# Kernel optimization log

Hardware: AMD Instinct MI355X
Metric: run time of the kernel (lower is better)

Reference implementation:

```python
import jax, jax.numpy as jnp
import numpy as np
import math

B, N, L = 1, 256, 384
D_MSA, D_PAIR, H, DH = 256, 128, 8, 32
EPS = 1e-5


def layernorm(x, g, b):
    mu = jnp.mean(x, axis=-1, keepdims=True)
    var = jnp.mean(jnp.square(x - mu), axis=-1, keepdims=True)
    return (x - mu) * jax.lax.rsqrt(var + EPS) * g + b


def setup_inputs() -> dict:
    key = jax.random.key(0)
    ks = jax.random.split(key, 16)
    s_msa = 1.0 / math.sqrt(D_MSA)
    s_pair = 1.0 / math.sqrt(D_PAIR)
    s_hd = 1.0 / math.sqrt(H * DH)
    return {
        "msa": jax.random.normal(ks[0], (B, N, L, D_MSA), jnp.float32),
        "pair": jax.random.normal(ks[1], (B, L, L, D_PAIR), jnp.float32),
        "ln_msa_g": jnp.ones((D_MSA,), jnp.float32),
        "ln_msa_b": jnp.zeros((D_MSA,), jnp.float32),
        "ln_pair_g": jnp.ones((D_PAIR,), jnp.float32),
        "ln_pair_b": jnp.zeros((D_PAIR,), jnp.float32),
        # SequenceWeight projections (stored as (in, out): y = x @ W + b)
        "Wq_sw": jax.random.normal(ks[2], (D_MSA, H * DH), jnp.float32) * s_msa,
        "bq_sw": jnp.zeros((H * DH,), jnp.float32),
        "Wk_sw": jax.random.normal(ks[3], (D_MSA, H * DH), jnp.float32) * s_msa,
        "bk_sw": jnp.zeros((H * DH,), jnp.float32),
        # Main attention projections (bias-free q/k/v)
        "Wq": jax.random.normal(ks[4], (D_MSA, H * DH), jnp.float32) * s_msa,
        "Wk": jax.random.normal(ks[5], (D_MSA, H * DH), jnp.float32) * s_msa,
        "Wv": jax.random.normal(ks[6], (D_MSA, H * DH), jnp.float32) * s_msa,
        "Wb": jax.random.normal(ks[7], (D_PAIR, H), jnp.float32) * s_pair,
        "Wg": jax.random.normal(ks[8], (D_MSA, H * DH), jnp.float32) * s_msa,
        "bg": jnp.ones((H * DH,), jnp.float32),
        "Wo": jax.random.normal(ks[9], (H * DH, D_MSA), jnp.float32) * s_hd,
        "bo": jnp.zeros((D_MSA,), jnp.float32),
    }


def reference(msa, pair, ln_msa_g, ln_msa_b, ln_pair_g, ln_pair_b,
              Wq_sw, bq_sw, Wk_sw, bk_sw, Wq, Wk, Wv, Wb, Wg, bg, Wo, bo):
    b, n, l, _ = msa.shape
    scale = 1.0 / math.sqrt(DH)

    m = layernorm(msa, ln_msa_g, ln_msa_b)  # (B,N,L,d_msa)

    # --- SequenceWeight: per-sequence, per-position, per-head weights ---
    q_sw = (m[:, 0] @ Wq_sw + bq_sw).reshape(b, l, H, DH) * scale   # (B,L,h,d)
    k_sw = (m @ Wk_sw + bk_sw).reshape(b, n, l, H, DH)              # (B,N,L,h,d)
    sw_logits = jnp.einsum('bihd,bnihd->bnih', q_sw, k_sw)
    seq_weight = jax.nn.softmax(sw_logits, axis=1)[..., None]       # (B,N,L,h,1)

    # --- Row attention with pair bias ---
    q = (m @ Wq).reshape(b, n, l, H, DH) * seq_weight               # seq-weighted queries
    k = (m @ Wk).reshape(b, n, l, H, DH) * scale
    logits = jnp.einsum('bnihd,bnjhd->bijh', q, k)                  # sum over N and d
    bias = layernorm(pair, ln_pair_g, ln_pair_b) @ Wb               # (B,L,L,h)
    attn = jax.nn.softmax(logits + bias, axis=2)                    # softmax over j

    v = (m @ Wv).reshape(b, n, l, H, DH)
    out = jnp.einsum('bijh,bnjhd->bnihd', attn, v).reshape(b, n, l, H * DH)

    gate = jax.nn.sigmoid(m @ Wg + bg)
    return (out * gate) @ Wo + bo                                   # (B,N,L,d_msa)
```

## Files before the change

### kernel.cpp

```cpp
#include <hip/hip_runtime.h>
#include <stdint.h>

#define NSEQ 256
#define LRES 384
#define NH   8
#define NL   (NSEQ*LRES)
#define SCALE 0.17677669529663687f

typedef unsigned short u16;
typedef unsigned int   u32;
typedef short bf16x8 __attribute__((ext_vector_type(8)));
typedef float f32x4  __attribute__((ext_vector_type(4)));

__device__ __forceinline__ u16 f2bf(float f) {
    u32 x = __float_as_uint(f);
    return (u16)((x + 0x7fffu + ((x >> 16) & 1u)) >> 16);
}
__device__ __forceinline__ u32 pack2(float a, float b) {
    u32 xa = __float_as_uint(a);
    u32 xb = __float_as_uint(b);
    xa = (xa + 0x7fffu + ((xa >> 16) & 1u)) >> 16;
    xb = ((xb + 0x7fffu + ((xb >> 16) & 1u)) >> 16) << 16;
    return xa | xb;
}
__device__ __forceinline__ uint4 pack8(const float f[8]) {
    uint4 r;
    r.x = pack2(f[0], f[1]); r.y = pack2(f[2], f[3]);
    r.z = pack2(f[4], f[5]); r.w = pack2(f[6], f[7]);
    return r;
}
__device__ __forceinline__ void unpack2(u32 u, float& f0, float& f1) {
    f0 = __uint_as_float((u & 0xffffu) << 16);
    f1 = __uint_as_float(u & 0xffff0000u);
}
__device__ __forceinline__ void unpack8(uint4 p, float f[8]) {
    unpack2(p.x, f[0], f[1]);
    unpack2(p.y, f[2], f[3]);
    unpack2(p.z, f[4], f[5]);
    unpack2(p.w, f[6], f[7]);
}

__device__ __forceinline__ float wred_sum(float v) {
#pragma unroll
    for (int o = 32; o > 0; o >>= 1) v += __shfl_xor(v, o, 64);
    return v;
}
__device__ __forceinline__ float wred_max(float v) {
#pragma unroll
    for (int o = 32; o > 0; o >>= 1) v = fmaxf(v, __shfl_xor(v, o, 64));
    return v;
}

__global__ __launch_bounds__(256) void ln_msa_k(
    const float* __restrict__ x, const float* __restrict__ g,
    const float* __restrict__ b, u16* __restrict__ lnA,
    float* __restrict__ stats)
{
    const int lane = threadIdx.x & 63;
    const int row = blockIdx.x * 4 + (threadIdx.x >> 6);
    const size_t base = (size_t)row * 256 + lane * 4;
    float4 v = *(const float4*)(x + base);
    float s  = wred_sum(v.x + v.y + v.z + v.w);
    float sq = wred_sum(v.x*v.x + v.y*v.y + v.z*v.z + v.w*v.w);
    const float mu  = s * (1.f / 256.f);
    const float var = sq * (1.f / 256.f) - mu * mu;
    const float rs  = rsqrtf(var + 1e-5f);
    if (lane == 0) {
        stats[(size_t)row * 2]     = mu;
        stats[(size_t)row * 2 + 1] = rs;
    }
    float4 gg = *(const float4*)(g + lane * 4);
    float4 bb = *(const float4*)(b + lane * 4);
    float f0 = (v.x - mu) * rs * gg.x + bb.x;
    float f1 = (v.y - mu) * rs * gg.y + bb.y;
    float f2 = (v.z - mu) * rs * gg.z + bb.z;
    float f3 = (v.w - mu) * rs * gg.w + bb.w;
    uint2 pk;
    pk.x = pack2(f0, f1);
    pk.y = pack2(f2, f3);
    *(uint2*)(lnA + base) = pk;
}

__global__ __launch_bounds__(256) void wconv_k(
    const float* __restrict__ W0, const float* __restrict__ W1,
    const float* __restrict__ W2, const float* __restrict__ W3,
    const float* __restrict__ W4, const float* __restrict__ W5,
    u16* __restrict__ outAll)
{
    const float* Wsrc[6] = {W0, W1, W2, W3, W4, W5};
    const int widx = blockIdx.x >> 4;
    const int tile = blockIdx.x & 15;
    const int kt = tile >> 2, ct = tile & 3;
    const float* W = Wsrc[widx];
    __shared__ float ts[64][65];
    const int r  = threadIdx.x >> 2;
    const int cg = threadIdx.x & 3;
#pragma unroll
    for (int jj = 0; jj < 4; ++jj) {
        float4 v = *(const float4*)(W + (size_t)(kt * 64 + r) * 256
                                      + ct * 64 + cg * 16 + jj * 4);
        ts[r][cg * 16 + jj * 4 + 0] = v.x;
        ts[r][cg * 16 + jj * 4 + 1] = v.y;
        ts[r][cg * 16 + jj * 4 + 2] = v.z;
        ts[r][cg * 16 + jj * 4 + 3] = v.w;
    }
    __syncthreads();
    float lo[8], hi[8];
#pragma unroll
    for (int j = 0; j < 8; ++j) lo[j] = ts[cg * 16 + j][r];
#pragma unroll
    for (int j = 0; j < 8; ++j) hi[j] = ts[cg * 16 + 8 + j][r];
    u16* o = outAll + (size_t)widx * 65536 + (size_t)(ct * 64 + r) * 256
           + kt * 64 + cg * 16;
    *(uint4*)(o)     = pack8(lo);
    *(uint4*)(o + 8) = pack8(hi);
}

__global__ __launch_bounds__(128) void wbprep_k(
    const float* __restrict__ g, const float* __restrict__ b,
    const float* __restrict__ Wb, float* __restrict__ Wp,
    float* __restrict__ AB)
{
    __shared__ float ps[128][8];
    __shared__ float pb[128][8];
    const int c = threadIdx.x;
    const float gc = g[c], bc = b[c];
    float4 w0 = *(const float4*)(Wb + (size_t)c * 8);
    float4 w1 = *(const float4*)(Wb + (size_t)c * 8 + 4);
    const float wraw[8] = {w0.x, w0.y, w0.z, w0.w, w1.x, w1.y, w1.z, w1.w};
    float wp[8];
#pragma unroll
    for (int h = 0; h < 8; ++h) {
        wp[h] = wraw[h] * gc;
        ps[c][h] = wp[h];
        pb[c][h] = wraw[h] * bc;
    }
    *(float4*)(Wp + (size_t)c * 8)     = make_float4(wp[0], wp[1], wp[2], wp[3]);
    *(float4*)(Wp + (size_t)c * 8 + 4) = make_float4(wp[4], wp[5], wp[6], wp[7]);
    __syncthreads();
    if (c < 8) {
        float a = 0.f;
        for (int j = 0; j < 128; ++j) a += ps[j][c];
        AB[c] = a;
    } else if (c < 16) {
        const int h = c - 8;
        float a = 0.f;
        for (int j = 0; j < 128; ++j) a += pb[j][h];
        AB[8 + h] = a;
    }
}

__global__ __launch_bounds__(256) void gemm_ln_k(
    const void* __restrict__ Av, int a_bf16,
    const float* __restrict__ stats,
    const float* __restrict__ lng, const float* __restrict__ lnb,
    const float* __restrict__ W, const float* __restrict__ bias,
    void* __restrict__ out, const float* __restrict__ seqw, int mode)
{
    __shared__ float As_t[32][68];
    __shared__ float Ws[32][132];
    __shared__ float gs[256], bs[256];
    const int tid = threadIdx.x;
    const int bx = blockIdx.y;
    const int by = blockIdx.x;
    const int tx = tid & 15, ty = tid >> 4;
    const int ar = tid >> 2, acg = tid & 3;
    const int wr = tid >> 3, wcg = tid & 7;
    const bool do_ln = (stats != nullptr);

    if (do_ln) { gs[tid] = lng[tid]; bs[tid] = lnb[tid]; }
    __syncthreads();

    const int arow_idx = by * 64 + ar;
    float mu = 0.f, rsg = 0.f;
    if (do_ln) {
        mu  = stats[(size_t)arow_idx * 2];
        rsg = stats[(size_t)arow_idx * 2 + 1];
    }

    float acc[4][8];
#pragma unroll
    for (int i = 0; i < 4; ++i)
#pragma unroll
        for (int j = 0; j < 8; ++j) acc[i][j] = 0.f;

    const size_t arow = (size_t)arow_idx * 256 + acg * 8;

    for (int kk = 0; kk < 256; kk += 32) {
        float af[8];
        if (a_bf16) {
            uint4 a8 = *(const uint4*)((const u16*)Av + arow + kk);
            unpack8(a8, af);
        } else {
            float4 x0 = *(const float4*)((const float*)Av + arow + kk);
            float4 x1 = *(const float4*)((const float*)Av + arow + kk + 4);
            af[0] = x0.x; af[1] = x0.y; af[2] = x0.z; af[3] = x0.w;
            af[4] = x1.x; af[5] = x1.y; af[6] = x1.z; af[7] = x1.w;
        }
        const float* wrow = W + (size_t)(kk + wr) * 256 + bx * 128 + wcg * 16;
        float4 w0 = *(const float4*)(wrow);
        float4 w1 = *(const float4*)(wrow + 4);
        float4 w2 = *(const float4*)(wrow + 8);
        float4 w3 = *(const float4*)(wrow + 12);
        if (do_ln) {
#pragma unroll
            for (int j = 0; j < 8; ++j) {
                const int k = kk + acg * 8 + j;
                af[j] = (af[j] - mu) * rsg * gs[k] + bs[k];
            }
        }
        __syncthreads();
#pragma unroll
        for (int j = 0; j < 8; ++j) As_t[acg * 8 + j][ar] = af[j];
        float* wsrow = &Ws[wr][wcg * 16];
        *(float4*)(wsrow)      = w0;
        *(float4*)(wsrow + 4)  = w1;
        *(float4*)(wsrow + 8)  = w2;
        *(float4*)(wsrow + 12) = w3;
        __syncthreads();
#pragma unroll 8
        for (int k = 0; k < 32; ++k) {
            const float4 a  = *(const float4*)&As_t[k][ty * 4];
            const float4 b0 = *(const float4*)&Ws[k][tx * 8];
            const float4 b1 = *(const float4*)&Ws[k][tx * 8 + 4];
            const float av[4] = {a.x, a.y, a.z, a.w};
            const float bv[8] = {b0.x, b0.y, b0.z, b0.w, b1.x, b1.y, b1.z, b1.w};
#pragma unroll
            for (int i = 0; i < 4; ++i)
#pragma unroll
                for (int j = 0; j < 8; ++j)
                    acc[i][j] = fmaf(av[i], bv[j], acc[i][j]);
        }
    }

    const int gc0 = bx * 128 + tx * 8;
    float bias8[8];
#pragma unroll
    for (int j = 0; j < 8; ++j) bias8[j] = bias[gc0 + j];

    float* o = (float*)out;
#pragma unroll
    for (int i = 0; i < 4; ++i) {
        const size_t gr = (size_t)by * 64 + ty * 4 + i;
#pragma unroll
        for (int j = 0; j < 8; ++j)
            o[gr * 256 + gc0 + j] = (acc[i][j] + bias8[j]) * SCALE;
    }
}

__global__ __launch_bounds__(256) void softmax_n_k(float* __restrict__ swl)
{
    const int col = blockIdx.x * 4 + (threadIdx.x >> 6);
    const int lane = threadIdx.x & 63;
    float* base = swl + col;
    float v[4];
#pragma unroll
    for (int t = 0; t < 4; ++t) v[t] = base[(size_t)(lane * 4 + t) * 3072];
    float mx = wred_max(fmaxf(fmaxf(v[0], v[1]), fmaxf(v[2], v[3])));
    float e[4], s = 0.f;
#pragma unroll
    for (int t = 0; t < 4; ++t) { e[t] = __expf(v[t] - mx); s += e[t]; }
    s = wred_sum(s);
    const float inv = 1.f / s;
#pragma unroll
    for (int t = 0; t < 4; ++t) base[(size_t)(lane * 4 + t) * 3072] = e[t] * inv;
}

__global__ __launch_bounds__(256) void pair_bias_k(
    const float* __restrict__ pairX, const float* __restrict__ Wp,
    const float* __restrict__ AB, float* __restrict__ biasH)
{
    __shared__ float ws[128][8];
    __shared__ float As[8], Bs[8];
    const int tid = threadIdx.x;
    {
        float4 w4 = *(const float4*)(Wp + tid * 4);
        *(float4*)(&ws[tid >> 1][(tid & 1) * 4]) = w4;
    }
    if (tid < 8)       As[tid] = AB[tid];
    else if (tid < 16) Bs[tid - 8] = AB[tid];
    __syncthreads();

    const int lane = tid & 63;
    const int p  = lane >> 3;
    const int cg = lane & 7;
    const size_t pb = (size_t)blockIdx.x * 32 + (tid >> 6) * 8 + p;
    const float* src = pairX + pb * 128 + cg * 16;
    float x[16];
    *(float4*)(x)      = *(const float4*)(src);
    *(float4*)(x + 4)  = *(const float4*)(src + 4);
    *(float4*)(x + 8)  = *(const float4*)(src + 8);
    *(float4*)(x + 12) = *(const float4*)(src + 12);

    float s = 0.f, sq = 0.f;
#pragma unroll
    for (int j = 0; j < 16; ++j) { s += x[j]; sq += x[j] * x[j]; }
#pragma unroll
    for (int o = 1; o <= 4; o <<= 1) {
        s  += __shfl_xor(s, o, 64);
        sq += __shfl_xor(sq, o, 64);
    }
    const float mu  = s * (1.f / 128.f);
    const float var = sq * (1.f / 128.f) - mu * mu;
    const float rs  = rsqrtf(var + 1e-5f);

    float acc[8];
#pragma unroll
    for (int hh = 0; hh < 8; ++hh) {
        const int h = hh ^ cg;
        float a = 0.f;
#pragma unroll
        for (int j = 0; j < 16; ++j) a += x[j] * ws[cg * 16 + j][h];
        acc[hh] = a;
    }
#pragma unroll
    for (int o = 1; o <= 4; o <<= 1) {
        float nv[8];
#pragma unroll
        for (int hh = 0; hh < 8; ++hh)
            nv[hh] = acc[hh] + __shfl_xor(acc[hh ^ o], o, 64);
#pragma unroll
        for (int hh = 0; hh < 8; ++hh) acc[hh] = nv[hh];
    }
    const float res = rs * acc[0] - rs * mu * As[cg] + Bs[cg];
    biasH[pb * 8 + cg] = res;
}

__device__ __forceinline__ void stage128x64(
    const u16* __restrict__ src, size_t rowStride, u16* lds, int tid)
{
    const int row   = tid >> 1;
    const int cbase = (tid & 1) * 4;
#pragma unroll
    for (int ch = 0; ch < 4; ++ch) {
        const int cc = cbase + ch;
        const uint4 v = *(const uint4*)(src + (size_t)row * rowStride + cc * 8);
        *(uint4*)(lds + row * 64 + ((cc ^ (row & 7)) * 8)) = v;
    }
}

__device__ __forceinline__ bf16x8 frag_read(const u16* lds, int row, int kchunk)
{
    return *(const bf16x8*)(lds + row * 64 + ((kchunk ^ (row & 7)) * 8));
}

__device__ __forceinline__ void proj_core(
    const u16* __restrict__ Ab, const u16* __restrict__ Wb,
    u16* tA, u16* tW, int tid, int mrow, int nrow, int g, f32x4 acc[4][4])
{
#pragma unroll
    for (int m = 0; m < 4; ++m)
#pragma unroll
        for (int n = 0; n < 4; ++n) {
            f32x4 z = {0.f, 0.f, 0.f, 0.f};
            acc[m][n] = z;
        }
    for (int k0 = 0; k0 < 256; k0 += 64) {
        stage128x64(Ab + k0, 256, tA, tid);
        stage128x64(Wb + k0, 256, tW, tid);
        __syncthreads();
#pragma unroll
        for (int ks = 0; ks < 2; ++ks) {
            bf16x8 wf[4], af[4];
#pragma unroll
            for (int m = 0; m < 4; ++m) wf[m] = frag_read(tW, mrow + m * 16, ks * 4 + g);
#pragma unroll
            for (int n = 0; n < 4; ++n) af[n] = frag_read(tA, nrow + n * 16, ks * 4 + g);
#pragma unroll
            for (int m = 0; m < 4; ++m)
#pragma unroll
                for (int n = 0; n < 4; ++n)
                    acc[m][n] = __builtin_amdgcn_mfma_f32_16x16x32_bf16(
                        wf[m], af[n], acc[m][n], 0, 0, 0);
        }
        __syncthreads();
    }
}

__global__ __launch_bounds__(256) void proj4_mfma(
    const u16* __restrict__ A,
    const u16* __restrict__ Wt_ksw, const u16* __restrict__ Wt_k,
    const u16* __restrict__ Wt_v,   const u16* __restrict__ Wt_g,
    const float* __restrict__ bias_ksw, const float* __restrict__ bias_g,
    const float* __restrict__ qsw,
    float* __restrict__ swl, u16* __restrict__ outKT,
    u16* __restrict__ outVT, u16* __restrict__ outGATE)
{
    __shared__ u16 tA[128 * 64];
    __shared__ u16 tW[128 * 64];

    int wg = (blockIdx.x & 7) * 192 + (blockIdx.x >> 3);
    const int rowTile = wg >> 1;
    const int colTile = wg & 1;

    const int tid  = threadIdx.x;
    const int lane = tid & 63, wid = tid >> 6;
    const int wr = wid >> 1, wc = wid & 1;
    const int g  = lane >> 4;
    const int mrow = wr * 64 + (lane & 15);
    const int nrow = wc * 64 + (lane & 15);

    const u16* Ab = A + (size_t)rowTile * 128 * 256;
    const size_t woff = (size_t)colTile * 128 * 256;

    const int cq0 = colTile * 128 + wr * 64 + ((lane >> 4) << 2);
    const int r0  = rowTile * 128 + wc * 64 + (lane & 15);

    f32x4 acc[4][4];

    proj_core(Ab, Wt_ksw + woff, tA, tW, tid, mrow, nrow, g, acc);
    {
        const int hbase = (colTile * 128 + wr * 64) >> 5;
#pragma unroll
        for (int n = 0; n < 4; ++n) {
            const int r = r0 + n * 16;
            const int ii = r % LRES;
            float s0 = 0.f, s1 = 0.f;
#pragma unroll
            for (int m = 0; m < 4; ++m) {
                const int c = cq0 + m * 16;
                const float4 b4 = *(const float4*)(bias_ksw + c);
                const float4 q4 = *(const float4*)(qsw + (size_t)ii * 256 + c);
                const f32x4 a = acc[m][n];
                const float part = (a[0] + b4.x) * q4.x + (a[1] + b4.y) * q4.y
                                 + (a[2] + b4.z) * q4.z + (a[3] + b4.w) * q4.w;
                if (m < 2) s0 += part; else s1 += part;
            }
            s0 += __shfl_xor(s0, 16, 64); s0 += __shfl_xor(s0, 32, 64);
            s1 += __shfl_xor(s1, 16, 64); s1 += __shfl_xor(s1, 32, 64);
            if (lane < 16) {
                swl[(size_t)r * 8 + hbase]     = s0;
                swl[(size_t)r * 8 + hbase + 1] = s1;
            }
        }
    }

    proj_core(Ab, Wt_k + woff, tA, tW, tid, mrow, nrow, g, acc);
#pragma unroll
    for (int m = 0; m < 4; ++m) {
        const int c = cq0 + m * 16;
        const int h = c >> 5, d = c & 31;
#pragma unroll
        for (int n = 0; n < 4; ++n) {
            const int r = r0 + n * 16;
            const int n_ = r / LRES, ii = r % LRES;
            const f32x4 a = acc[m][n];
            uint2 pk;
            pk.x = pack2(a[0] * SCALE, a[1] * SCALE);
            pk.y = pack2(a[2] * SCALE, a[3] * SCALE);
            *(uint2*)(outKT + (size_t)h * 3145728
                      + (size_t)ii * 8192 + n_ * 32 + d) = pk;
        }
    }

    proj_core(Ab, Wt_v + woff, tA, tW, tid, mrow, nrow, g, acc);
#pragma unroll
    for (int m = 0; m < 4; ++m) {
        const int c = cq0 + m * 16;
        const int h = c >> 5, d = c & 31;
#pragma unroll
        for (int n = 0; n < 4; ++n) {
            const int r = r0 + n * 16;
            const int n_ = r / LRES, ii = r % LRES;
            const f32x4 a = acc[m][n];
            u16* o = outVT + (size_t)h * 3145728
                   + (size_t)(n_ * 32 + d) * 384 + ii;
            o[0]    = f2bf(a[0]);
            o[384]  = f2bf(a[1]);
            o[768]  = f2bf(a[2]);
            o[1152] = f2bf(a[3]);
        }
    }

    proj_core(Ab, Wt_g + woff, tA, tW, tid, mrow, nrow, g, acc);
#pragma unroll
    for (int m = 0; m < 4; ++m) {
        const int c = cq0 + m * 16;
        const float4 b4 = *(const float4*)(bias_g + c);
#pragma unroll
        for (int n = 0; n < 4; ++n) {
            const int r = r0 + n * 16;
            const f32x4 a = acc[m][n];
            const float f0 = 1.f / (1.f + __expf(-(a[0] + b4.x)));
            const float f1 = 1.f / (1.f + __expf(-(a[1] + b4.y)));
            const float f2 = 1.f / (1.f + __expf(-(a[2] + b4.z)));
            const float f3 = 1.f / (1.f + __expf(-(a[3] + b4.w)));
            uint2 pk;
            pk.x = pack2(f0, f1);
            pk.y = pack2(f2, f3);
            *(uint2*)(outGATE + (size_t)r * 256 + c) = pk;
        }
    }
}

enum { PROJ_QT = 1, PROJ_OUT = 5 };

__global__ __launch_bounds__(256) void proj_mfma(
    const u16* __restrict__ A, const u16* __restrict__ Wt,
    const float* __restrict__ bias, const float* __restrict__ seqw,
    void* __restrict__ out, int mode)
{
    __shared__ u16 tA[128 * 64];
    __shared__ u16 tW[128 * 64];

    int wg = (blockIdx.x & 7) * 192 + (blockIdx.x >> 3);
    const int rowTile = wg >> 1;
    const int colTile = wg & 1;

    const int tid  = threadIdx.x;
    const int lane = tid & 63, wid = tid >> 6;
    const int wr = wid >> 1, wc = wid & 1;
    const int g  = lane >> 4;
    const int mrow = wr * 64 + (lane & 15);
    const int nrow = wc * 64 + (lane & 15);

    f32x4 acc[4][4];
    proj_core(A + (size_t)rowTile * 128 * 256, Wt + (size_t)colTile * 128 * 256,
              tA, tW, tid, mrow, nrow, g, acc);

    const int cq0 = colTile * 128 + wr * 64 + ((lane >> 4) << 2);
    const int r0  = rowTile * 128 + wc * 64 + (lane & 15);

#pragma unroll
    for (int m = 0; m < 4; ++m) {
        const int c = cq0 + m * 16;
#pragma unroll
        for (int n = 0; n < 4; ++n) {
            const int r = r0 + n * 16;
            const f32x4 a = acc[m][n];
            if (mode == PROJ_QT) {
                const int h = c >> 5, d = c & 31;
                const int n_ = r / LRES, ii = r % LRES;
                const float mult = seqw[(size_t)r * NH + h];
                uint2 pk;
                pk.x = pack2(a[0] * mult, a[1] * mult);
                pk.y = pack2(a[2] * mult, a[3] * mult);
                *(uint2*)((u16*)out + (size_t)h * 3145728
                          + (size_t)ii * 8192 + n_ * 32 + d) = pk;
            } else {
                float* o = (float*)out + (size_t)r * 256 + c;
                o[0] = a[0] + bias[c];
                o[1] = a[1] + bias[c + 1];
                o[2] = a[2] + bias[c + 2];
                o[3] = a[3] + bias[c + 3];
            }
        }
    }
}

__global__ __launch_bounds__(256) void gemm_logits_mfma(
    const u16* __restrict__ qT, const u16* __restrict__ kT,
    float* __restrict__ part)
{
    __shared__ u16 tQ[128 * 64];
    __shared__ u16 tK[128 * 64];

    int wg = (blockIdx.x & 7) * 36 + (blockIdx.x >> 3);
    const int gsel = wg / 9;
    const int t    = wg % 9;
    const int h  = gsel >> 2, kc = gsel & 3;
    const int bi = t / 3, bj = t % 3;

    const u16* Q = qT + (size_t)h * 3145728 + (size_t)bi * 128 * 8192;
    const u16* K = kT + (size_t)h * 3145728 + (size_t)bj * 128 * 8192;

    const int tid  = threadIdx.x;
    const int lane = tid & 63, wid = tid >> 6;
    const int wr = wid >> 1, wc = wid & 1;
    const int g  = lane >> 4;
    const int mrow = wr * 64 + (lane & 15);
    const int nrow = wc * 64 + (lane & 15);

    f32x4 acc[4][4];
#pragma unroll
    for (int m = 0; m < 4; ++m)
#pragma unroll
        for (int n = 0; n < 4; ++n) {
            f32x4 z = {0.f, 0.f, 0.f, 0.f};
            acc[m][n] = z;
        }

    const int k0beg = kc * 2048, k0end = k0beg + 2048;
    for (int k0 = k0beg; k0 < k0end; k0 += 64) {
        stage128x64(Q + k0, 8192, tQ, tid);
        stage128x64(K + k0, 8192, tK, tid);
        __syncthreads();
#pragma unroll
        for (int ks = 0; ks < 2; ++ks) {
            bf16x8 kf[4], qf[4];
#pragma unroll
            for (int m = 0; m < 4; ++m) kf[m] = frag_read(tK, mrow + m * 16, ks * 4 + g);
#pragma unroll
            for (int n = 0; n < 4; ++n) qf[n] = frag_read(tQ, nrow + n * 16, ks * 4 + g);
#pragma unroll
            for (int m = 0; m < 4; ++m)
#pragma unroll
                for (int n = 0; n < 4; ++n)
                    acc[m][n] = __builtin_amdgcn_mfma_f32_16x16x32_bf16(
                        kf[m], qf[n], acc[m][n], 0, 0, 0);
        }
        __syncthreads();
    }

    float* dst = part + (size_t)kc * 1179648 + (size_t)h * 147456;
    const int gj_base = bj * 128 + wr * 64 + ((lane >> 4) << 2);
    const int gi_base = bi * 128 + wc * 64 + (lane & 15);
#pragma unroll
    for (int m = 0; m < 4; ++m)
#pragma unroll
        for (int n = 0; n < 4; ++n) {
            const int gi = gi_base + n * 16;
            const int gj = gj_base + m * 16;
            *(f32x4*)(dst + (size_t)gi * 384 + gj) = acc[m][n];
        }
}

__global__ __launch_bounds__(256) void softmax_j_k(
    const float* __restrict__ part, const float* __restrict__ biasH,
    u16* __restrict__ attnB)
{
    const int row = blockIdx.x * 4 + (threadIdx.x >> 6);
    const int lane = threadIdx.x & 63;
    const int h = row / LRES, i = row % LRES;
    const float* p = part + (size_t)h * 147456 + (size_t)i * 384;
    const float* bh = biasH + (size_t)i * 3072 + h;
    float v[6];
#pragma unroll
    for (int t = 0; t < 6; ++t) {
        const int j = t * 64 + lane;
        v[t] = p[j] + p[j + 1179648] + p[j + 2359296] + p[j + 3538944]
             + bh[(size_t)j * 8];
    }
    float mx = v[0];
#pragma unroll
    for (int t = 1; t < 6; ++t) mx = fmaxf(mx, v[t]);
    mx = wred_max(mx);
    float e[6], s = 0.f;
#pragma unroll
    for (int t = 0; t < 6; ++t) { e[t] = __expf(v[t] - mx); s += e[t]; }
    s = wred_sum(s);
    const float inv = 1.f / s;
    u16* ab = attnB + (size_t)h * 147456 + (size_t)i * 384;
#pragma unroll
    for (int t = 0; t < 6; ++t) ab[t * 64 + lane] = f2bf(e[t] * inv);
}

__global__ __launch_bounds__(256) void gemm_out_mfma(
    const u16* __restrict__ attnB, const u16* __restrict__ vTT,
    u16* gate_io)
{
    __shared__ u16 tV[128 * 64];
    __shared__ u16 tA[128 * 64];

    int wg = (blockIdx.x & 7) * 192 + (blockIdx.x >> 3);
    const int h  = wg / 192;
    const int r  = wg % 192;
    const int bn = r / 3;
    const int bi = r % 3;

    const u16* A = attnB + (size_t)h * 147456 + (size_t)bi * 128 * 384;
    const u16* V = vTT   + (size_t)h * 3145728 + (size_t)bn * 128 * 384;

    const int tid  = threadIdx.x;
    const int lane = tid & 63, wid = tid >> 6;
    const int wr = wid >> 1, wc = wid & 1;
    const int g  = lane >> 4;
    const int mrow = wr * 64 + (lane & 15);
    const int nrow = wc * 64 + (lane & 15);

    f32x4 acc[4][4];
#pragma unroll
    for (int m = 0; m < 4; ++m)
#pragma unroll
        for (int n = 0; n < 4; ++n) {
            f32x4 z = {0.f, 0.f, 0.f, 0.f};
            acc[m][n] = z;
        }

    for (int j0 = 0; j0 < 384; j0 += 64) {
        stage128x64(V + j0, 384, tV, tid);
        stage128x64(A + j0, 384, tA, tid);
        __syncthreads();
#pragma unroll
        for (int ks = 0; ks < 2; ++ks) {
            bf16x8 vf[4], af[4];
#pragma unroll
            for (int m = 0; m < 4; ++m) vf[m] = frag_read(tV, mrow + m * 16, ks * 4 + g);
#pragma unroll
            for (int n = 0; n < 4; ++n) af[n] = frag_read(tA, nrow + n * 16, ks * 4 + g);
#pragma unroll
            for (int m = 0; m < 4; ++m)
#pragma unroll
                for (int n = 0; n < 4; ++n)
                    acc[m][n] = __builtin_amdgcn_mfma_f32_16x16x32_bf16(
                        vf[m], af[n], acc[m][n], 0, 0, 0);
        }
        __syncthreads();
    }

    const int nd_base = bn * 128 + wr * 64 + ((lane >> 4) << 2);
    const int i_base  = bi * 128 + wc * 64 + (lane & 15);
#pragma unroll
    for (int m = 0; m < 4; ++m) {
        const int nd = nd_base + m * 16;
        const int nseq = nd >> 5, d = nd & 31;
#pragma unroll
        for (int n = 0; n < 4; ++n) {
            const int gi = i_base + n * 16;
            const size_t addr = ((size_t)(nseq * LRES + gi)) * 256 + h * 32 + d;
            uint2 g2 = *(const uint2*)(gate_io + addr);
            float gf[4];
            unpack2(g2.x, gf[0], gf[1]);
            unpack2(g2.y, gf[2], gf[3]);
            const f32x4 a = acc[m][n];
            uint2 pk;
            pk.x = pack2(a[0] * gf[0], a[1] * gf[1]);
            pk.y = pack2(a[2] * gf[2], a[3] * gf[3]);
            *(uint2*)(gate_io + addr) = pk;
        }
    }
}

extern "C" void kernel_launch(void* const* d_in, const int* in_sizes, int n_in,
                              void* d_out, int out_size, void* d_ws, size_t ws_size,
                              hipStream_t stream)
{
    const float* msa       = (const float*)d_in[0];
    const float* pair      = (const float*)d_in[1];
    const float* ln_msa_g  = (const float*)d_in[2];
    const float* ln_msa_b  = (const float*)d_in[3];
    const float* ln_pair_g = (const float*)d_in[4];
    const float* ln_pair_b = (const float*)d_in[5];
    const float* Wq_sw     = (const float*)d_in[6];
    const float* bq_sw     = (const float*)d_in[7];
    const float* Wk_sw     = (const float*)d_in[8];
    const float* bk_sw     = (const float*)d_in[9];
    const float* Wq        = (const float*)d_in[10];
    const float* Wk        = (const float*)d_in[11];
    const float* Wv        = (const float*)d_in[12];
    const float* Wb        = (const float*)d_in[13];
    const float* Wg        = (const float*)d_in[14];
    const float* bg        = (const float*)d_in[15];
    const float* Wo        = (const float*)d_in[16];
    const float* bo        = (const float*)d_in[17];
    float* out = (float*)d_out;

    char* ws = (char*)d_ws;
    u16*   B0 = (u16*)(ws + 0);
    u16*   B1 = (u16*)(ws + 50331648);
    u16*   B2 = (u16*)(ws + 100663296);
    u16*   B3 = (u16*)(ws + 150994944);
    u16*   lnA = (u16*)(ws + 201326592);
    float* part  = (float*)(ws + 201326592);
    u16*   attnB = (u16*)(ws + 201326592 + 18874368);
    float* biasH = (float*)(ws + 201326592 + 21233664);
    float* stats = (float*)(ws + 251658240);
    float* qsw   = (float*)(ws + 252444672);
    float* swl   = (float*)(ws + 252837888);
    u16*   WtAll = (u16*)(ws + 255983616);
    float* Wp    = (float*)(ws + 256770048);
    float* AB    = (float*)(ws + 256774144);

    u16* Wt_ksw = WtAll;
    u16* Wt_q   = WtAll + 65536;
    u16* Wt_k   = WtAll + 131072;
    u16* Wt_v   = WtAll + 196608;
    u16* Wt_g   = WtAll + 262144;
    u16* Wt_o   = WtAll + 327680;

    ln_msa_k<<<NL / 4, 256, 0, stream>>>(msa, ln_msa_g, ln_msa_b, lnA, stats);
    wconv_k<<<96, 256, 0, stream>>>(Wk_sw, Wq, Wk, Wv, Wg, Wo, WtAll);
    wbprep_k<<<1, 128, 0, stream>>>(ln_pair_g, ln_pair_b, Wb, Wp, AB);
    gemm_ln_k<<<dim3(LRES / 64, 2), 256, 0, stream>>>(
        msa, 0, stats, ln_msa_g, ln_msa_b, Wq_sw, bq_sw, qsw, nullptr, 1);
    proj4_mfma<<<1536, 256, 0, stream>>>(
        lnA, Wt_ksw, Wt_k, Wt_v, Wt_g, bk_sw, bg, qsw, swl, B1, B2, B3);
    softmax_n_k<<<LRES * NH / 4, 256, 0, stream>>>(swl);
    proj_mfma<<<1536, 256, 0, stream>>>(lnA, Wt_q, nullptr, swl, B0, PROJ_QT);
    pair_bias_k<<<LRES * LRES / 32, 256, 0, stream>>>(pair, Wp, AB, biasH);
    gemm_logits_mfma<<<288, 256, 0, stream>>>(B0, B1, part);
    softmax_j_k<<<NH * LRES / 4, 256, 0, stream>>>(part, biasH, attnB);
    gemm_out_mfma<<<1536, 256, 0, stream>>>(attnB, B2, B3);
    proj_mfma<<<1536, 256, 0, stream>>>(B3, Wt_o, bo, nullptr, out, PROJ_OUT);
}
```

Before: 662.9 us.

## Split fused four-projection kernel into one workgroup per weight slot

Before, each workgroup ran four back-to-back GEMMs over the same A row tile (k_sw, k, v, gate). Now the grid is four times larger and each workgroup computes a single projection, picked by a slot index, with a branch for the matching epilogue. Weights are reordered so the four projections sit next to each other and one base pointer plus a slot offset reaches them. The aim is more parallelism, shorter per-workgroup latency and better occupancy via launch_bounds(256,4), at the cost of loading each A tile four times instead of reusing it.

Measured after the change: 605.3 us. 8.7% less time.

```diff
diff --git a/kernel.cpp b/kernel.cpp
--- a/kernel.cpp
+++ b/kernel.cpp
@@ -377,10 +377,8 @@
     }
 }
 
-__global__ __launch_bounds__(256) void proj4_mfma(
-    const u16* __restrict__ A,
-    const u16* __restrict__ Wt_ksw, const u16* __restrict__ Wt_k,
-    const u16* __restrict__ Wt_v,   const u16* __restrict__ Wt_g,
+__global__ __launch_bounds__(256, 4) void projX_mfma(
+    const u16* __restrict__ A, const u16* __restrict__ Wt4,
     const float* __restrict__ bias_ksw, const float* __restrict__ bias_g,
     const float* __restrict__ qsw,
     float* __restrict__ swl, u16* __restrict__ outKT,
@@ -389,8 +387,9 @@
     __shared__ u16 tA[128 * 64];
     __shared__ u16 tW[128 * 64];
 
-    int wg = (blockIdx.x & 7) * 192 + (blockIdx.x >> 3);
-    const int rowTile = wg >> 1;
+    int wg = (blockIdx.x & 7) * 768 + (blockIdx.x >> 3);
+    const int rowTile = wg >> 3;
+    const int slot    = (wg >> 1) & 3;
     const int colTile = wg & 1;
 
     const int tid  = threadIdx.x;
@@ -401,15 +400,15 @@
     const int nrow = wc * 64 + (lane & 15);
 
     const u16* Ab = A + (size_t)rowTile * 128 * 256;
-    const size_t woff = (size_t)colTile * 128 * 256;
+    const u16* Wb = Wt4 + (size_t)slot * 65536 + (size_t)colTile * 128 * 256;
+
+    f32x4 acc[4][4];
+    proj_core(Ab, Wb, tA, tW, tid, mrow, nrow, g, acc);
 
     const int cq0 = colTile * 128 + wr * 64 + ((lane >> 4) << 2);
     const int r0  = rowTile * 128 + wc * 64 + (lane & 15);
 
-    f32x4 acc[4][4];
-
-    proj_core(Ab, Wt_ksw + woff, tA, tW, tid, mrow, nrow, g, acc);
-    {
+    if (slot == 0) {
         const int hbase = (colTile * 128 + wr * 64) >> 5;
 #pragma unroll
         for (int n = 0; n < 4; ++n) {
@@ -433,62 +432,59 @@
                 swl[(size_t)r * 8 + hbase + 1] = s1;
             }
         }
-    }
-
-    proj_core(Ab, Wt_k + woff, tA, tW, tid, mrow, nrow, g, acc);
-#pragma unroll
-    for (int m = 0; m < 4; ++m) {
-        const int c = cq0 + m * 16;
-        const int h = c >> 5, d = c & 31;
-#pragma unroll
-        for (int n = 0; n < 4; ++n) {
-            const int r = r0 + n * 16;
-            const int n_ = r / LRES, ii = r % LRES;
-            const f32x4 a = acc[m][n];
-            uint2 pk;
-            pk.x = pack2(a[0] * SCALE, a[1] * SCALE);
-            pk.y = pack2(a[2] * SCALE, a[3] * SCALE);
-            *(uint2*)(outKT + (size_t)h * 3145728
-                      + (size_t)ii * 8192 + n_ * 32 + d) = pk;
-        }
-    }
-
-    proj_core(Ab, Wt_v + woff, tA, tW, tid, mrow, nrow, g, acc);
-#pragma unroll
-    for (int m = 0; m < 4; ++m) {
-        const int c = cq0 + m * 16;
-        const int h = c >> 5, d = c & 31;
-#pragma unroll
-        for (int n = 0; n < 4; ++n) {
-            const int r = r0 + n * 16;
-            const int n_ = r / LRES, ii = r % LRES;
-            const f32x4 a = acc[m][n];
-            u16* o = outVT + (size_t)h * 3145728
-                   + (size_t)(n_ * 32 + d) * 384 + ii;
-            o[0]    = f2bf(a[0]);
-            o[384]  = f2bf(a[1]);
-            o[768]  = f2bf(a[2]);
-            o[1152] = f2bf(a[3]);
-        }
-    }
-
-    proj_core(Ab, Wt_g + woff, tA, tW, tid, mrow, nrow, g, acc);
-#pragma unroll
-    for (int m = 0; m < 4; ++m) {
-        const int c = cq0 + m * 16;
-        const float4 b4 = *(const float4*)(bias_g + c);
-#pragma unroll
-        for (int n = 0; n < 4; ++n) {
-            const int r = r0 + n * 16;
-            const f32x4 a = acc[m][n];
-            const float f0 = 1.f / (1.f + __expf(-(a[0] + b4.x)));
-            const float f1 = 1.f / (1.f + __expf(-(a[1] + b4.y)));
-            const float f2 = 1.f / (1.f + __expf(-(a[2] + b4.z)));
-            const float f3 = 1.f / (1.f + __expf(-(a[3] + b4.w)));
-            uint2 pk;
-            pk.x = pack2(f0, f1);
-            pk.y = pack2(f2, f3);
-            *(uint2*)(outGATE + (size_t)r * 256 + c) = pk;
+    } else if (slot == 1) {
+#pragma unroll
+        for (int m = 0; m < 4; ++m) {
+            const int c = cq0 + m * 16;
+            const int h = c >> 5, d = c & 31;
+#pragma unroll
+            for (int n = 0; n < 4; ++n) {
+                const int r = r0 + n * 16;
+                const int n_ = r / LRES, ii = r % LRES;
+                const f32x4 a = acc[m][n];
+                uint2 pk;
+                pk.x = pack2(a[0] * SCALE, a[1] * SCALE);
+                pk.y = pack2(a[2] * SCALE, a[3] * SCALE);
+                *(uint2*)(outKT + (size_t)h * 3145728
+                          + (size_t)ii * 8192 + n_ * 32 + d) = pk;
+            }
+        }
+    } else if (slot == 2) {
+#pragma unroll
+        for (int m = 0; m < 4; ++m) {
+            const int c = cq0 + m * 16;
+            const int h = c >> 5, d = c & 31;
+#pragma unroll
+            for (int n = 0; n < 4; ++n) {
+                const int r = r0 + n * 16;
+                const int n_ = r / LRES, ii = r % LRES;
+                const f32x4 a = acc[m][n];
+                u16* o = outVT + (size_t)h * 3145728
+                       + (size_t)(n_ * 32 + d) * 384 + ii;
+                o[0]    = f2bf(a[0]);
+                o[384]  = f2bf(a[1]);
+                o[768]  = f2bf(a[2]);
+                o[1152] = f2bf(a[3]);
+            }
+        }
+    } else {
+#pragma unroll
+        for (int m = 0; m < 4; ++m) {
+            const int c = cq0 + m * 16;
+            const float4 b4 = *(const float4*)(bias_g + c);
+#pragma unroll
+            for (int n = 0; n < 4; ++n) {
+                const int r = r0 + n * 16;
+                const f32x4 a = acc[m][n];
+                const float f0 = 1.f / (1.f + __expf(-(a[0] + b4.x)));
+                const float f1 = 1.f / (1.f + __expf(-(a[1] + b4.y)));
+                const float f2 = 1.f / (1.f + __expf(-(a[2] + b4.z)));
+                const float f3 = 1.f / (1.f + __expf(-(a[3] + b4.w)));
+                uint2 pk;
+                pk.x = pack2(f0, f1);
+                pk.y = pack2(f2, f3);
+                *(uint2*)(outGATE + (size_t)r * 256 + c) = pk;
+            }
         }
     }
 }
@@ -761,20 +757,16 @@
     float* Wp    = (float*)(ws + 256770048);
     float* AB    = (float*)(ws + 256774144);
 
-    u16* Wt_ksw = WtAll;
-    u16* Wt_q   = WtAll + 65536;
-    u16* Wt_k   = WtAll + 131072;
-    u16* Wt_v   = WtAll + 196608;
-    u16* Wt_g   = WtAll + 262144;
-    u16* Wt_o   = WtAll + 327680;
+    u16* Wt_q   = WtAll + 4 * 65536;
+    u16* Wt_o   = WtAll + 5 * 65536;
 
     ln_msa_k<<<NL / 4, 256, 0, stream>>>(msa, ln_msa_g, ln_msa_b, lnA, stats);
-    wconv_k<<<96, 256, 0, stream>>>(Wk_sw, Wq, Wk, Wv, Wg, Wo, WtAll);
+    wconv_k<<<96, 256, 0, stream>>>(Wk_sw, Wk, Wv, Wg, Wq, Wo, WtAll);
     wbprep_k<<<1, 128, 0, stream>>>(ln_pair_g, ln_pair_b, Wb, Wp, AB);
     gemm_ln_k<<<dim3(LRES / 64, 2), 256, 0, stream>>>(
         msa, 0, stats, ln_msa_g, ln_msa_b, Wq_sw, bq_sw, qsw, nullptr, 1);
-    proj4_mfma<<<1536, 256, 0, stream>>>(
-        lnA, Wt_ksw, Wt_k, Wt_v, Wt_g, bk_sw, bg, qsw, swl, B1, B2, B3);
+    projX_mfma<<<6144, 256, 0, stream>>>(
+        lnA, WtAll, bk_sw, bg, qsw, swl, B1, B2, B3);
     softmax_n_k<<<LRES * NH / 4, 256, 0, stream>>>(swl);
     proj_mfma<<<1536, 256, 0, stream>>>(lnA, Wt_q, nullptr, swl, B0, PROJ_QT);
     pair_bias_k<<<LRES * LRES / 32, 256, 0, stream>>>(pair, Wp, AB, biasH);
```
